# Kernel optimization log

Hardware: AMD Instinct MI355X
Metric: run time of the kernel (lower is better)

## Reference

```python
import jax, jax.numpy as jnp
import numpy as np

DIM = 1024
HEADS = 16
DIM_HEAD = 64
B, N = 2, 2048
EPS_NORM = 1e-12  # F.normalize clamp


def setup_inputs() -> dict:
    key = jax.random.key(0)
    k1, k2, k3 = jax.random.split(key, 3)
    x = jax.random.normal(k1, (B, N, DIM), dtype=jnp.float32)
    gamma = jnp.ones((DIM,), dtype=jnp.float32)
    w_qkv = jax.random.normal(k2, (DIM, 3 * HEADS * DIM_HEAD), dtype=jnp.float32) * (DIM ** -0.5)
    w_out = jax.random.normal(k3, (HEADS * DIM_HEAD, DIM), dtype=jnp.float32) * (DIM ** -0.5)
    return {"x": x, "gamma": gamma, "w_qkv": w_qkv, "w_out": w_out}


def reference(x, gamma, w_qkv, w_out):
    b, n, dim = x.shape
    h, dh = HEADS, DIM_HEAD
    # RMSNorm: F.normalize(x, dim=-1) * sqrt(dim) * gamma
    norm = jnp.maximum(jnp.linalg.norm(x, axis=-1, keepdims=True), EPS_NORM)
    normed = x / norm * (dim ** 0.5) * gamma
    # qkv projection (no bias)
    qkv = normed @ w_qkv  # [b, n, 3*h*dh]
    qkv = qkv.reshape(b, n, 3, h, dh)
    q = qkv[:, :, 0].transpose(0, 2, 1, 3)  # [b, h, n, dh]
    k = qkv[:, :, 1].transpose(0, 2, 1, 3)
    v = qkv[:, :, 2].transpose(0, 2, 1, 3)
    q = q * (dh ** -0.5)
    # attention scores
    sim = jnp.einsum('bhid,bhjd->bhij', q, k)
    mask_value = -jnp.finfo(sim.dtype).max
    # causal mask: triu with offset j - i + 1 (here i == j == n -> offset 1)
    causal_mask = jnp.triu(jnp.ones((n, n), dtype=bool), 1)
    sim = jnp.where(causal_mask, mask_value, sim)
    attn = jax.nn.softmax(sim, axis=-1)
    out = jnp.einsum('bhij,bhjd->bhid', attn, v)
    out = out.transpose(0, 2, 1, 3).reshape(b, n, h * dh)
    return out @ w_out
```

## Files before the change

kernel.cpp:

```cpp
#include <hip/hip_runtime.h>
#include <hip/hip_bf16.h>

typedef unsigned short u16;
using bf16x8 = __attribute__((ext_vector_type(8))) short;
using f32x4  = __attribute__((ext_vector_type(4))) float;
using f32x16 = __attribute__((ext_vector_type(16))) float;
using u32x4  = __attribute__((ext_vector_type(4))) unsigned int;

constexpr int B_ = 2, N_ = 2048, DIM_ = 1024, H_ = 16, DH_ = 64;
constexpr int M_ = B_ * N_;
constexpr int NCQ = 3 * H_ * DH_;

__device__ inline u16 f2bf(float f) {
  union { float f; unsigned u; } v{f};
  unsigned r = v.u + 0x7FFF + ((v.u >> 16) & 1);
  return (u16)(r >> 16);
}

__device__ __forceinline__ void st_pair(u16* p0, u16* p1, float a, float b) {
  unsigned w;
  asm("v_cvt_pk_bf16_f32 %0, %1, %2" : "=v"(w) : "v"(a), "v"(b));
  *p0 = (u16)w;
  *p1 = (u16)(w >> 16);
}

__device__ __forceinline__ void gload16(const u16* g, u16* l) {
  __builtin_amdgcn_global_load_lds(
      (const __attribute__((address_space(1))) unsigned int*)g,
      (__attribute__((address_space(3))) unsigned int*)l, 16, 0, 0);
}

__global__ void __launch_bounds__(256) rmsnorm_kernel(const float* __restrict__ x,
                                                      const float* __restrict__ gamma,
                                                      u16* __restrict__ out) {
  int row = blockIdx.x;
  int t = threadIdx.x;
  const float4 v = reinterpret_cast<const float4*>(x + (size_t)row * DIM_)[t];
  float ss = v.x * v.x + v.y * v.y + v.z * v.z + v.w * v.w;
#pragma unroll
  for (int o = 32; o; o >>= 1) ss += __shfl_down(ss, o, 64);
  __shared__ float partial[4];
  int wid = t >> 6, lane = t & 63;
  if (lane == 0) partial[wid] = ss;
  __syncthreads();
  float tot = partial[0] + partial[1] + partial[2] + partial[3];
  float norm = fmaxf(sqrtf(tot), 1e-12f);
  float scale = 32.0f / norm;
  const float4 g = reinterpret_cast<const float4*>(gamma)[t];
  ushort4 o4;
  o4.x = f2bf(v.x * scale * g.x);
  o4.y = f2bf(v.y * scale * g.y);
  o4.z = f2bf(v.z * scale * g.z);
  o4.w = f2bf(v.w * scale * g.w);
  reinterpret_cast<ushort4*>(out + (size_t)row * DIM_)[t] = o4;
}

__global__ void __launch_bounds__(256) transpose_w_kernel(const float* __restrict__ W,
                                                          u16* __restrict__ WT,
                                                          int K, int Nc) {
  __shared__ float tile[32][33];
  int bc = blockIdx.x * 32;
  int bk = blockIdx.y * 32;
  int tx = threadIdx.x & 31, ty = threadIdx.x >> 5;
#pragma unroll
  for (int r = ty; r < 32; r += 8)
    tile[r][tx] = W[(size_t)(bk + r) * Nc + bc + tx];
  __syncthreads();
#pragma unroll
  for (int r = ty; r < 32; r += 8)
    WT[(size_t)(bc + r) * K + bk + tx] = f2bf(tile[tx][r]);
}

template <int MODE>
__global__ void __launch_bounds__(256) gemm2_kernel(const u16* __restrict__ A,
                                                    const u16* __restrict__ BT,
                                                    void* __restrict__ Cv,
                                                    u16* __restrict__ q_s,
                                                    u16* __restrict__ k_s,
                                                    u16* __restrict__ vq,
                                                    int M, int Nc, int K) {
  __shared__ alignas(16) u16 abuf[2][4096];
  __shared__ alignas(16) u16 bbuf[2][4096];
  int tid = threadIdx.x;
  int lane = tid & 63, wid = tid >> 6;
  int lr = lane & 15, g = lane >> 4;
  int am0 = (wid >> 1) * 64;
  int bn0 = (wid & 1) * 64;
  int rbase_a = blockIdx.y * 128;
  int rbase_b = blockIdx.x * 128;

  int lineo = tid >> 3;
  int p = tid & 7;
  f32x4 acc[4][4] = {};

#define GSTAGE(buf_, src_, rb_, k0_) do {                                            \
    _Pragma("unroll")                                                                \
    for (int c = 0; c < 2; c++) {                                                    \
      int line = c * 32 + lineo;                                                     \
      int sp = p ^ (line & 7);                                                       \
      int row = 2 * line + (sp >> 2);                                                \
      int j = sp & 3;                                                                \
      gload16(src_ + (size_t)(rb_ + row) * K + (k0_) + j * 8,                        \
              &buf_[c * 2048 + wid * 512]);                                          \
    }                                                                                \
  } while (0)

#define STAGE(ib_, k0_) do {                                                         \
    GSTAGE(abuf[ib_], A, rbase_a, k0_);                                              \
    GSTAGE(bbuf[ib_], BT, rbase_b, k0_);                                             \
  } while (0)

  int steps = K >> 5;
  STAGE(0, 0);
  for (int t = 0; t < steps; ++t) {
    int ibuf = t & 1;
    if (t + 1 < steps) {
      STAGE(ibuf ^ 1, (t + 1) * 32);
      asm volatile("s_waitcnt vmcnt(4)" ::: "memory");
    } else {
      asm volatile("s_waitcnt vmcnt(0)" ::: "memory");
    }
    __builtin_amdgcn_s_barrier();
    __builtin_amdgcn_sched_barrier(0);

    const char* ab = (const char*)abuf[ibuf];
    const char* bb = (const char*)bbuf[ibuf];
    bf16x8 a[4], b[4];
#pragma unroll
    for (int mi = 0; mi < 4; mi++) {
      int row = am0 + mi * 16 + lr;
      int byte = (row >> 1) * 128 + ((((row & 1) << 2) + g) ^ ((row >> 1) & 7)) * 16;
      a[mi] = *reinterpret_cast<const bf16x8*>(ab + byte);
    }
#pragma unroll
    for (int ni = 0; ni < 4; ni++) {
      int row = bn0 + ni * 16 + lr;
      int byte = (row >> 1) * 128 + ((((row & 1) << 2) + g) ^ ((row >> 1) & 7)) * 16;
      b[ni] = *reinterpret_cast<const bf16x8*>(bb + byte);
    }
#pragma unroll
    for (int mi = 0; mi < 4; mi++)
#pragma unroll
      for (int ni = 0; ni < 4; ni++)
        acc[mi][ni] = __builtin_amdgcn_mfma_f32_16x16x32_bf16(a[mi], b[ni], acc[mi][ni], 0, 0, 0);

    __builtin_amdgcn_sched_barrier(0);
    __builtin_amdgcn_s_barrier();
  }

  int orow = g * 4;
  if (MODE == 1) {
#pragma unroll
    for (int mi = 0; mi < 4; mi++)
#pragma unroll
      for (int ni = 0; ni < 4; ni++)
#pragma unroll
        for (int r = 0; r < 4; r++) {
          int row = rbase_a + am0 + 16 * mi + orow + r;
          int col = rbase_b + bn0 + 16 * ni + lr;
          ((float*)Cv)[(size_t)row * Nc + col] = acc[mi][ni][r];
        }
  } else {
    int colbase = rbase_b + bn0;
    int region = colbase >> 10;
    int head = (colbase >> 6) & 15;
    const float QS = 0.125f * 1.4426950408889634f;
#pragma unroll
    for (int mi = 0; mi < 4; mi++)
#pragma unroll
      for (int ni = 0; ni < 4; ni++)
#pragma unroll
        for (int r = 0; r < 4; r += 2) {
          int row = rbase_a + am0 + 16 * mi + orow + r;
          int n = row & 2047, bb_ = row >> 11;
          float v0 = acc[mi][ni][r], v1 = acc[mi][ni][r + 1];
          if (region == 0) {
            size_t d0 = ((size_t)(bb_ * 16 + head) * 2048 + n) * 64 + 16 * ni + lr;
            st_pair(q_s + d0, q_s + d0 + 64, v0 * QS, v1 * QS);
          } else if (region == 1) {
            size_t d0 = ((size_t)(bb_ * 16 + head) * 2048 + n) * 64 + 16 * ni + lr;
            st_pair(k_s + d0, k_s + d0 + 64, v0, v1);
          } else {
            size_t d0 = (size_t)row * 1024 + (colbase - 2048) + 16 * ni + lr;
            st_pair(vq + d0, vq + d0 + 1024, v0, v1);
          }
        }
  }
#undef STAGE
#undef GSTAGE
}

__global__ void __launch_bounds__(256) transpose_v_kernel(const u16* __restrict__ Vq,
                                                          u16* __restrict__ vt) {
  __shared__ u16 tile[64][65];
  int blk = blockIdx.x;
  int nt = blk & 31;
  int bh = blk >> 5;
  int h = bh & 15, b = bh >> 4;
  int n0 = nt * 64;
  int tx = threadIdx.x & 15, ty = threadIdx.x >> 4;
#pragma unroll
  for (int r = ty; r < 64; r += 16) {
    ushort4 v4 = *reinterpret_cast<const ushort4*>(
        Vq + (size_t)(b * N_ + n0 + r) * 1024 + h * 64 + tx * 4);
    tile[r][tx * 4 + 0] = v4.x;
    tile[r][tx * 4 + 1] = v4.y;
    tile[r][tx * 4 + 2] = v4.z;
    tile[r][tx * 4 + 3] = v4.w;
  }
  __syncthreads();
#pragma unroll
  for (int r = ty; r < 64; r += 16) {
    ushort4 o4;
    o4.x = tile[tx * 4 + 0][r];
    o4.y = tile[tx * 4 + 1][r];
    o4.z = tile[tx * 4 + 2][r];
    o4.w = tile[tx * 4 + 3][r];
    *reinterpret_cast<ushort4*>(vt + ((size_t)(b * H_ + h) * DH_ + r) * N_ + n0 + tx * 4) = o4;
  }
}

__global__ void __launch_bounds__(256) attn5_kernel(const u16* __restrict__ q_s,
                                                    const u16* __restrict__ k_s,
                                                    const u16* __restrict__ vt,
                                                    u16* __restrict__ ao) {
  __shared__ alignas(16) u16 smem[16384];
  u16* kb0 = smem;
  u16* vb0 = smem + 8192;
  int tid = threadIdx.x;
  int lane = tid & 63, wid = tid >> 6;
  int q31 = lane & 31, hi = lane >> 5;
  int strip = wid >> 1, myhalf = wid & 1;
  int blk = blockIdx.x;
  int bh = blk & 31;
  int j = 31 - (blk >> 5);
  int b = bh >> 4, h = bh & 15;
  const u16* qp = q_s + (size_t)bh * N_ * DH_;
  const u16* kp = k_s + (size_t)bh * N_ * DH_;
  const u16* vp = vt + (size_t)bh * DH_ * N_;
  int q0w = j * 64 + strip * 32;
  int qi = q0w + q31;
  int steps = j + 1;

  bf16x8 qf[4];
#pragma unroll
  for (int c = 0; c < 4; c++)
    qf[c] = *reinterpret_cast<const bf16x8*>(qp + (size_t)(q0w + q31) * 64 + c * 16 + hi * 8);

  f32x16 o0 = {}, o1 = {};
  float lsum = 0.f;

  int srow = lane >> 3;
  int scol = (lane & 7) ^ srow;
  int c0 = wid * 2, c1 = c0 + 1;

#define STAGE(ibuf_, kv0_) do {                                                              \
    gload16(kp + (size_t)((kv0_) + c0 * 8 + srow) * 64 + scol * 8,                           \
            kb0 + (ibuf_) * 4096 + c0 * 512);                                                \
    gload16(kp + (size_t)((kv0_) + c1 * 8 + srow) * 64 + scol * 8,                           \
            kb0 + (ibuf_) * 4096 + c1 * 512);                                                \
    gload16(vp + (size_t)(c0 * 8 + srow) * N_ + (kv0_) + scol * 8,                           \
            vb0 + (ibuf_) * 4096 + c0 * 512);                                                \
    gload16(vp + (size_t)(c1 * 8 + srow) * N_ + (kv0_) + scol * 8,                           \
            vb0 + (ibuf_) * 4096 + c1 * 512);                                                \
  } while (0)

  STAGE(0, 0);

  for (int t = 0; t < steps; ++t) {
    int ibuf = t & 1;
    if (t + 1 < steps) {
      STAGE(ibuf ^ 1, (t + 1) * 64);
      asm volatile("s_waitcnt vmcnt(4)" ::: "memory");
    } else {
      asm volatile("s_waitcnt vmcnt(0)" ::: "memory");
    }
    __builtin_amdgcn_s_barrier();
    __builtin_amdgcn_sched_barrier(0);

    const u16* kb = kb0 + ibuf * 4096;
    const u16* vb = vb0 + ibuf * 4096;
    int kv = t * 64 + myhalf * 32;
    if (kv <= q0w + 31) {
      f32x16 st = {};
      int krow = myhalf * 32 + q31;
      int ksw = (krow & 7) << 4;
      __builtin_amdgcn_s_setprio(1);
#pragma unroll
      for (int c = 0; c < 4; c++) {
        bf16x8 kf = *reinterpret_cast<const bf16x8*>(
            (const char*)kb + krow * 128 + (((c * 2 + hi) * 16) ^ ksw));
        st = __builtin_amdgcn_mfma_f32_32x32x16_bf16(kf, qf[c], st, 0, 0, 0);
      }
      __builtin_amdgcn_s_setprio(0);
      float p[16];
      bool diag = (kv + 31 > q0w);
      if (diag) {
#pragma unroll
        for (int r = 0; r < 16; r++) {
          int key = kv + (r & 3) + 8 * (r >> 2) + 4 * hi;
          float e = __builtin_amdgcn_exp2f(st[r]);
          p[r] = (key > qi) ? 0.f : e;
        }
      } else {
#pragma unroll
        for (int r = 0; r < 16; r++) p[r] = __builtin_amdgcn_exp2f(st[r]);
      }
#pragma unroll
      for (int r = 0; r < 16; r++) lsum += p[r];
      unsigned cw0[4], cw1[4];
#pragma unroll
      for (int jq = 0; jq < 4; jq++) {
        asm("v_cvt_pk_bf16_f32 %0, %1, %2" : "=v"(cw0[jq]) : "v"(p[4 * jq]), "v"(p[4 * jq + 1]));
        asm("v_cvt_pk_bf16_f32 %0, %1, %2" : "=v"(cw1[jq]) : "v"(p[4 * jq + 2]), "v"(p[4 * jq + 3]));
      }
#pragma unroll
      for (int kc = 0; kc < 2; kc++) {
        unsigned c0a = cw0[2 * kc], c0b = cw0[2 * kc + 1];
        unsigned c1a = cw1[2 * kc], c1b = cw1[2 * kc + 1];
        unsigned sel0 = hi ? c0a : c0b;
        unsigned sel1 = hi ? c1a : c1b;
        unsigned r0 = (unsigned)__shfl_xor((int)sel0, 32, 64);
        unsigned r1 = (unsigned)__shfl_xor((int)sel1, 32, 64);
        u32x4 w;
        w[0] = hi ? r0 : c0a;
        w[1] = hi ? r1 : c1a;
        w[2] = hi ? c0b : r0;
        w[3] = hi ? c1b : r1;
        bf16x8 pa = __builtin_bit_cast(bf16x8, w);
        int slot = (myhalf * 4 + kc * 2 + hi) * 16;
        int vsw = (q31 & 7) << 4;
        bf16x8 vf0 = *reinterpret_cast<const bf16x8*>(
            (const char*)vb + q31 * 128 + (slot ^ vsw));
        bf16x8 vf1 = *reinterpret_cast<const bf16x8*>(
            (const char*)vb + (32 + q31) * 128 + (slot ^ vsw));
        __builtin_amdgcn_s_setprio(1);
        o0 = __builtin_amdgcn_mfma_f32_32x32x16_bf16(pa, vf0, o0, 0, 0, 0);
        o1 = __builtin_amdgcn_mfma_f32_32x32x16_bf16(pa, vf1, o1, 0, 0, 0);
        __builtin_amdgcn_s_setprio(0);
      }
    }
    __builtin_amdgcn_sched_barrier(0);
    __builtin_amdgcn_s_barrier();
  }

  __syncthreads();
  float lc = lsum + __shfl_xor(lsum, 32, 64);
  float* cb = (float*)smem;
  int pr = wid >> 1;
  if (myhalf) {
#pragma unroll
    for (int r = 0; r < 16; r++) {
      cb[pr * 2048 + r * 64 + lane] = o0[r];
      cb[pr * 2048 + (16 + r) * 64 + lane] = o1[r];
    }
    cb[4096 + pr * 64 + lane] = lc;
  }
  __syncthreads();
  if (!myhalf) {
#pragma unroll
    for (int r = 0; r < 16; r++) {
      o0[r] += cb[pr * 2048 + r * 64 + lane];
      o1[r] += cb[pr * 2048 + (16 + r) * 64 + lane];
    }
    float ltot = fmaxf(lc + cb[4096 + pr * 64 + lane], 1e-30f);
    float linv = 1.0f / ltot;
#pragma unroll
    for (int r = 0; r < 16; r += 2) {
      int qrow0 = (r & 3) + 8 * (r >> 2) + 4 * hi;
      float li0 = __shfl(linv, qrow0, 64);
      float li1 = __shfl(linv, qrow0 + 1, 64);
      size_t base0 = (size_t)(b * N_ + q0w + qrow0) * 1024 + h * 64;
      st_pair(ao + base0 + q31, ao + base0 + 1024 + q31, o0[r] * li0, o0[r + 1] * li1);
      st_pair(ao + base0 + 32 + q31, ao + base0 + 1024 + 32 + q31, o1[r] * li0, o1[r + 1] * li1);
    }
  }
#undef STAGE
}

extern "C" void kernel_launch(void* const* d_in, const int* in_sizes, int n_in,
                              void* d_out, int out_size, void* d_ws, size_t ws_size,
                              hipStream_t stream) {
  const float* x = (const float*)d_in[0];
  const float* gamma = (const float*)d_in[1];
  const float* w_qkv = (const float*)d_in[2];
  const float* w_out = (const float*)d_in[3];
  float* out = (float*)d_out;

  char* p = (char*)d_ws;
  u16* normed = (u16*)p; p += (size_t)M_ * DIM_ * 2;
  u16* wt_qkv = (u16*)p; p += (size_t)NCQ * DIM_ * 2;
  u16* wt_out = (u16*)p; p += (size_t)DIM_ * DIM_ * 2;
  u16* vq = (u16*)p;     p += (size_t)M_ * DIM_ * 2;
  u16* k_s = (u16*)p;    p += (size_t)M_ * DIM_ * 2;
  u16* vt = (u16*)p;     p += (size_t)M_ * DIM_ * 2;
  u16* q_s = (u16*)p;    p += (size_t)M_ * DIM_ * 2;
  u16* ao = vq;

  hipLaunchKernelGGL(rmsnorm_kernel, dim3(M_), dim3(256), 0, stream, x, gamma, normed);
  hipLaunchKernelGGL(transpose_w_kernel, dim3(NCQ / 32, DIM_ / 32), dim3(256), 0, stream,
                     w_qkv, wt_qkv, DIM_, NCQ);
  hipLaunchKernelGGL(transpose_w_kernel, dim3(DIM_ / 32, DIM_ / 32), dim3(256), 0, stream,
                     w_out, wt_out, DIM_, DIM_);
  hipLaunchKernelGGL(gemm2_kernel<2>, dim3(NCQ / 128, M_ / 128), dim3(256), 0, stream,
                     normed, wt_qkv, nullptr, q_s, k_s, vq, M_, NCQ, DIM_);
  hipLaunchKernelGGL(transpose_v_kernel, dim3(B_ * H_ * (N_ / 64)), dim3(256), 0, stream,
                     vq, vt);
  hipLaunchKernelGGL(attn5_kernel, dim3(B_ * H_ * (N_ / 64)), dim3(256), 0, stream,
                     q_s, k_s, vt, ao);
  hipLaunchKernelGGL(gemm2_kernel<1>, dim3(DIM_ / 128, M_ / 128), dim3(256), 0, stream,
                     ao, wt_out, (void*)out, nullptr, nullptr, nullptr, M_, DIM_, DIM_);
}
```

Before: 119.8 us.

## Fuse V transpose into QKV GEMM epilogue and triple-buffer attention K/V loads

```diff
diff --git a/kernel.cpp b/kernel.cpp
--- a/kernel.cpp
+++ b/kernel.cpp
@@ -77,10 +77,9 @@
                                                     void* __restrict__ Cv,
                                                     u16* __restrict__ q_s,
                                                     u16* __restrict__ k_s,
-                                                    u16* __restrict__ vq,
+                                                    u16* __restrict__ vt,
                                                     int M, int Nc, int K) {
-  __shared__ alignas(16) u16 abuf[2][4096];
-  __shared__ alignas(16) u16 bbuf[2][4096];
+  __shared__ alignas(16) u16 smem[16384];
   int tid = threadIdx.x;
   int lane = tid & 63, wid = tid >> 6;
   int lr = lane & 15, g = lane >> 4;
@@ -93,7 +92,7 @@
   int p = tid & 7;
   f32x4 acc[4][4] = {};
 
-#define GSTAGE(buf_, src_, rb_, k0_) do {                                            \
+#define GSTAGE(base_, src_, rb_, k0_) do {                                           \
     _Pragma("unroll")                                                                \
     for (int c = 0; c < 2; c++) {                                                    \
       int line = c * 32 + lineo;                                                     \
@@ -101,13 +100,13 @@
       int row = 2 * line + (sp >> 2);                                                \
       int j = sp & 3;                                                                \
       gload16(src_ + (size_t)(rb_ + row) * K + (k0_) + j * 8,                        \
-              &buf_[c * 2048 + wid * 512]);                                          \
+              (base_) + c * 2048 + wid * 512);                                       \
     }                                                                                \
   } while (0)
 
 #define STAGE(ib_, k0_) do {                                                         \
-    GSTAGE(abuf[ib_], A, rbase_a, k0_);                                              \
-    GSTAGE(bbuf[ib_], BT, rbase_b, k0_);                                             \
+    GSTAGE(smem + (ib_) * 4096, A, rbase_a, k0_);                                    \
+    GSTAGE(smem + 8192 + (ib_) * 4096, BT, rbase_b, k0_);                            \
   } while (0)
 
   int steps = K >> 5;
@@ -123,8 +122,8 @@
     __builtin_amdgcn_s_barrier();
     __builtin_amdgcn_sched_barrier(0);
 
-    const char* ab = (const char*)abuf[ibuf];
-    const char* bb = (const char*)bbuf[ibuf];
+    const char* ab = (const char*)(smem + ibuf * 4096);
+    const char* bb = (const char*)(smem + 8192 + ibuf * 4096);
     bf16x8 a[4], b[4];
 #pragma unroll
     for (int mi = 0; mi < 4; mi++) {
@@ -165,75 +164,69 @@
     int region = colbase >> 10;
     int head = (colbase >> 6) & 15;
     const float QS = 0.125f * 1.4426950408889634f;
-#pragma unroll
-    for (int mi = 0; mi < 4; mi++)
-#pragma unroll
-      for (int ni = 0; ni < 4; ni++)
-#pragma unroll
-        for (int r = 0; r < 4; r += 2) {
-          int row = rbase_a + am0 + 16 * mi + orow + r;
-          int n = row & 2047, bb_ = row >> 11;
-          float v0 = acc[mi][ni][r], v1 = acc[mi][ni][r + 1];
-          if (region == 0) {
+    if (region < 2) {
+#pragma unroll
+      for (int mi = 0; mi < 4; mi++)
+#pragma unroll
+        for (int ni = 0; ni < 4; ni++)
+#pragma unroll
+          for (int r = 0; r < 4; r += 2) {
+            int row = rbase_a + am0 + 16 * mi + orow + r;
+            int n = row & 2047, bb_ = row >> 11;
+            float v0 = acc[mi][ni][r], v1 = acc[mi][ni][r + 1];
             size_t d0 = ((size_t)(bb_ * 16 + head) * 2048 + n) * 64 + 16 * ni + lr;
-            st_pair(q_s + d0, q_s + d0 + 64, v0 * QS, v1 * QS);
-          } else if (region == 1) {
-            size_t d0 = ((size_t)(bb_ * 16 + head) * 2048 + n) * 64 + 16 * ni + lr;
-            st_pair(k_s + d0, k_s + d0 + 64, v0, v1);
-          } else {
-            size_t d0 = (size_t)row * 1024 + (colbase - 2048) + 16 * ni + lr;
-            st_pair(vq + d0, vq + d0 + 1024, v0, v1);
+            if (region == 0)
+              st_pair(q_s + d0, q_s + d0 + 64, v0 * QS, v1 * QS);
+            else
+              st_pair(k_s + d0, k_s + d0 + 64, v0, v1);
           }
+    } else {
+      u16* tlds = smem + wid * 4096;
+      int n_base = (rbase_a + am0) & 2047;
+      int bq = (rbase_a + am0) >> 11;
+#pragma unroll
+      for (int mi = 0; mi < 4; mi++)
+#pragma unroll
+        for (int ni = 0; ni < 4; ni++) {
+          int n_loc = mi * 16 + orow;
+          int dh_loc = ni * 16 + lr;
+          unsigned w0, w1;
+          asm("v_cvt_pk_bf16_f32 %0, %1, %2"
+              : "=v"(w0) : "v"(acc[mi][ni][0]), "v"(acc[mi][ni][1]));
+          asm("v_cvt_pk_bf16_f32 %0, %1, %2"
+              : "=v"(w1) : "v"(acc[mi][ni][2]), "v"(acc[mi][ni][3]));
+          int byte = dh_loc * 128 + ((n_loc * 2) ^ ((dh_loc & 7) << 4));
+          uint2 val; val.x = w0; val.y = w1;
+          *reinterpret_cast<uint2*>((char*)tlds + byte) = val;
         }
+#pragma unroll
+      for (int it = 0; it < 8; it++) {
+        int dh_loc = it * 8 + (lane >> 3);
+        int n8 = (lane & 7) * 8;
+        int byte = dh_loc * 128 + ((n8 * 2) ^ ((dh_loc & 7) << 4));
+        bf16x8 v = *reinterpret_cast<const bf16x8*>((const char*)tlds + byte);
+        size_t dst = ((size_t)(bq * 16 + head) * 64 + dh_loc) * 2048 + n_base + n8;
+        *reinterpret_cast<bf16x8*>(vt + dst) = v;
+      }
+    }
   }
 #undef STAGE
 #undef GSTAGE
 }
 
-__global__ void __launch_bounds__(256) transpose_v_kernel(const u16* __restrict__ Vq,
-                                                          u16* __restrict__ vt) {
-  __shared__ u16 tile[64][65];
-  int blk = blockIdx.x;
-  int nt = blk & 31;
-  int bh = blk >> 5;
-  int h = bh & 15, b = bh >> 4;
-  int n0 = nt * 64;
-  int tx = threadIdx.x & 15, ty = threadIdx.x >> 4;
-#pragma unroll
-  for (int r = ty; r < 64; r += 16) {
-    ushort4 v4 = *reinterpret_cast<const ushort4*>(
-        Vq + (size_t)(b * N_ + n0 + r) * 1024 + h * 64 + tx * 4);
-    tile[r][tx * 4 + 0] = v4.x;
-    tile[r][tx * 4 + 1] = v4.y;
-    tile[r][tx * 4 + 2] = v4.z;
-    tile[r][tx * 4 + 3] = v4.w;
-  }
-  __syncthreads();
-#pragma unroll
-  for (int r = ty; r < 64; r += 16) {
-    ushort4 o4;
-    o4.x = tile[tx * 4 + 0][r];
-    o4.y = tile[tx * 4 + 1][r];
-    o4.z = tile[tx * 4 + 2][r];
-    o4.w = tile[tx * 4 + 3][r];
-    *reinterpret_cast<ushort4*>(vt + ((size_t)(b * H_ + h) * DH_ + r) * N_ + n0 + tx * 4) = o4;
-  }
-}
-
-__global__ void __launch_bounds__(256) attn5_kernel(const u16* __restrict__ q_s,
+__global__ void __launch_bounds__(256) attn6_kernel(const u16* __restrict__ q_s,
                                                     const u16* __restrict__ k_s,
                                                     const u16* __restrict__ vt,
                                                     u16* __restrict__ ao) {
-  __shared__ alignas(16) u16 smem[16384];
-  u16* kb0 = smem;
-  u16* vb0 = smem + 8192;
+  __shared__ alignas(16) u16 smem[24576];
   int tid = threadIdx.x;
   int lane = tid & 63, wid = tid >> 6;
   int q31 = lane & 31, hi = lane >> 5;
   int strip = wid >> 1, myhalf = wid & 1;
   int blk = blockIdx.x;
   int bh = blk & 31;
-  int j = 31 - (blk >> 5);
+  int s = blk >> 5;
+  int j = (s & 1) ? (s >> 1) : (31 - (s >> 1));
   int b = bh >> 4, h = bh & 15;
   const u16* qp = q_s + (size_t)bh * N_ * DH_;
   const u16* kp = k_s + (size_t)bh * N_ * DH_;
@@ -254,23 +247,27 @@
   int scol = (lane & 7) ^ srow;
   int c0 = wid * 2, c1 = c0 + 1;
 
-#define STAGE(ibuf_, kv0_) do {                                                              \
+#define STAGE(rb_, kv0_) do {                                                                \
     gload16(kp + (size_t)((kv0_) + c0 * 8 + srow) * 64 + scol * 8,                           \
-            kb0 + (ibuf_) * 4096 + c0 * 512);                                                \
+            smem + (rb_) * 4096 + c0 * 512);                                                 \
     gload16(kp + (size_t)((kv0_) + c1 * 8 + srow) * 64 + scol * 8,                           \
-            kb0 + (ibuf_) * 4096 + c1 * 512);                                                \
+            smem + (rb_) * 4096 + c1 * 512);                                                 \
     gload16(vp + (size_t)(c0 * 8 + srow) * N_ + (kv0_) + scol * 8,                           \
-            vb0 + (ibuf_) * 4096 + c0 * 512);                                                \
+            smem + 12288 + (rb_) * 4096 + c0 * 512);                                         \
     gload16(vp + (size_t)(c1 * 8 + srow) * N_ + (kv0_) + scol * 8,                           \
-            vb0 + (ibuf_) * 4096 + c1 * 512);                                                \
+            smem + 12288 + (rb_) * 4096 + c1 * 512);                                         \
   } while (0)
 
   STAGE(0, 0);
-
+  if (steps > 1) STAGE(1, 64);
+
+  int cur = 0, pre = 2;
   for (int t = 0; t < steps; ++t) {
-    int ibuf = t & 1;
-    if (t + 1 < steps) {
-      STAGE(ibuf ^ 1, (t + 1) * 64);
+    if (t + 2 < steps) {
+      STAGE(pre, (t + 2) * 64);
+      pre = (pre == 2) ? 0 : pre + 1;
+      asm volatile("s_waitcnt vmcnt(8)" ::: "memory");
+    } else if (t + 1 < steps) {
       asm volatile("s_waitcnt vmcnt(4)" ::: "memory");
     } else {
       asm volatile("s_waitcnt vmcnt(0)" ::: "memory");
@@ -278,8 +275,9 @@
     __builtin_amdgcn_s_barrier();
     __builtin_amdgcn_sched_barrier(0);
 
-    const u16* kb = kb0 + ibuf * 4096;
-    const u16* vb = vb0 + ibuf * 4096;
+    const u16* kb = smem + cur * 4096;
+    const u16* vb = smem + 12288 + cur * 4096;
+    cur = (cur == 2) ? 0 : cur + 1;
     int kv = t * 64 + myhalf * 32;
     if (kv <= q0w + 31) {
       f32x16 st = {};
@@ -391,11 +389,10 @@
   u16* normed = (u16*)p; p += (size_t)M_ * DIM_ * 2;
   u16* wt_qkv = (u16*)p; p += (size_t)NCQ * DIM_ * 2;
   u16* wt_out = (u16*)p; p += (size_t)DIM_ * DIM_ * 2;
-  u16* vq = (u16*)p;     p += (size_t)M_ * DIM_ * 2;
   u16* k_s = (u16*)p;    p += (size_t)M_ * DIM_ * 2;
   u16* vt = (u16*)p;     p += (size_t)M_ * DIM_ * 2;
   u16* q_s = (u16*)p;    p += (size_t)M_ * DIM_ * 2;
-  u16* ao = vq;
+  u16* ao = (u16*)p;     p += (size_t)M_ * DIM_ * 2;
 
   hipLaunchKernelGGL(rmsnorm_kernel, dim3(M_), dim3(256), 0, stream, x, gamma, normed);
   hipLaunchKernelGGL(transpose_w_kernel, dim3(NCQ / 32, DIM_ / 32), dim3(256), 0, stream,
@@ -403,10 +400,8 @@
   hipLaunchKernelGGL(transpose_w_kernel, dim3(DIM_ / 32, DIM_ / 32), dim3(256), 0, stream,
                      w_out, wt_out, DIM_, DIM_);
   hipLaunchKernelGGL(gemm2_kernel<2>, dim3(NCQ / 128, M_ / 128), dim3(256), 0, stream,
-                     normed, wt_qkv, nullptr, q_s, k_s, vq, M_, NCQ, DIM_);
-  hipLaunchKernelGGL(transpose_v_kernel, dim3(B_ * H_ * (N_ / 64)), dim3(256), 0, stream,
-                     vq, vt);
-  hipLaunchKernelGGL(attn5_kernel, dim3(B_ * H_ * (N_ / 64)), dim3(256), 0, stream,
+                     normed, wt_qkv, nullptr, q_s, k_s, vt, M_, NCQ, DIM_);
+  hipLaunchKernelGGL(attn6_kernel, dim3(B_ * H_ * (N_ / 64)), dim3(256), 0, stream,
                      q_s, k_s, vt, ao);
   hipLaunchKernelGGL(gemm2_kernel<1>, dim3(DIM_ / 128, M_ / 128), dim3(256), 0, stream,
                      ao, wt_out, (void*)out, nullptr, nullptr, nullptr, M_, DIM_, DIM_);
```

After: 110.7 us. 1.08x faster.
